# Performance work log

Measured on AMD Instinct MI355X. Metric: run time of the kernel, lower is better.

Reference implementation:

```python
import jax, jax.numpy as jnp
import numpy as np

EPS_LN = 1e-5


def layer_norm(x, g, b):
    mu = jnp.mean(x, axis=-1, keepdims=True)
    var = jnp.mean((x - mu) ** 2, axis=-1, keepdims=True)
    return (x - mu) * jax.lax.rsqrt(var + EPS_LN) * g + b


def setup_inputs() -> dict:
    key = jax.random.key(0)
    ks = jax.random.split(key, 16)
    N, E, H, EA = 25000, 400000, 128, 1
    h = jax.random.normal(ks[0], (N, H), dtype=jnp.float32)
    coord = jax.random.normal(ks[1], (N, 3), dtype=jnp.float32)
    edge_index = jax.random.randint(ks[2], (2, E), 0, N, dtype=jnp.int64)
    edge_attr = jax.random.normal(ks[3], (E, EA), dtype=jnp.float32)

    def lin(k, fan_in, fan_out):
        lim = 1.0 / np.sqrt(fan_in)
        return jax.random.uniform(k, (fan_in, fan_out), jnp.float32, -lim, lim)

    in_edge = 2 * H + 1 + EA  # 258
    params = {
        'e_W1': lin(ks[4], in_edge, H), 'e_b1': jnp.zeros((H,), jnp.float32),
        'e_g1': jnp.ones((H,), jnp.float32), 'e_be1': jnp.zeros((H,), jnp.float32),
        'e_W2': lin(ks[5], H, H), 'e_b2': jnp.zeros((H,), jnp.float32),
        'e_g2': jnp.ones((H,), jnp.float32), 'e_be2': jnp.zeros((H,), jnp.float32),
        'n_W1': lin(ks[6], 2 * H, H), 'n_b1': jnp.zeros((H,), jnp.float32),
        'n_g1': jnp.ones((H,), jnp.float32), 'n_be1': jnp.zeros((H,), jnp.float32),
        'n_W2': lin(ks[7], H, H), 'n_b2': jnp.zeros((H,), jnp.float32),
        'c_W1': lin(ks[8], H, H), 'c_b1': jnp.zeros((H,), jnp.float32),
        'c_g1': jnp.ones((H,), jnp.float32), 'c_be1': jnp.zeros((H,), jnp.float32),
        # xavier_uniform with gain=0.001, no bias
        'c_W2': jax.random.uniform(ks[9], (H, 1), jnp.float32, -1.0, 1.0) * (0.001 * np.sqrt(6.0 / (H + 1))),
    }
    return dict(h=h, edge_index=edge_index, coord=coord, edge_attr=edge_attr, **params)


def reference(h, edge_index, coord, edge_attr,
              e_W1, e_b1, e_g1, e_be1, e_W2, e_b2, e_g2, e_be2,
              n_W1, n_b1, n_g1, n_be1, n_W2, n_b2,
              c_W1, c_b1, c_g1, c_be1, c_W2):
    N = h.shape[0]
    row, col = edge_index[0], edge_index[1]

    coord_diff = coord[row] - coord[col]                     # [E,3]
    radial = jnp.sum(coord_diff ** 2, axis=1, keepdims=True)  # [E,1]
    norm = jnp.sqrt(radial + 1e-8)
    coord_diff = coord_diff / (norm + 1.0)

    inp = jnp.concatenate([h[row], h[col], radial, edge_attr], axis=1)  # [E,258]
    x = jax.nn.silu(layer_norm(inp @ e_W1 + e_b1, e_g1, e_be1))
    edge_feat = jax.nn.silu(layer_norm(x @ e_W2 + e_b2, e_g2, e_be2))   # [E,H]

    cm = jax.nn.silu(layer_norm(edge_feat @ c_W1 + c_b1, c_g1, c_be1)) @ c_W2  # [E,1]
    trans = coord_diff * cm                                   # [E,3]

    coord_out = coord + jax.ops.segment_sum(trans, row, num_segments=N)
    agg = jax.ops.segment_sum(edge_feat, row, num_segments=N)  # [N,H]

    node_in = jnp.concatenate([h, agg], axis=1)               # [N,2H]
    out = jax.nn.silu(layer_norm(node_in @ n_W1 + n_b1, n_g1, n_be1)) @ n_W2 + n_b2
    out = h + out  # recurrent
    return out, coord_out
```

## Files before the change

kernel.cpp:

```cpp
#include <hip/hip_runtime.h>
#include <math.h>

#define H 128
#define KE 256
#define KN 256
#define XSTR 136

typedef __attribute__((ext_vector_type(8))) short bf16x8;
typedef __attribute__((ext_vector_type(4))) float f32x4;

__device__ __forceinline__ float silu_f(float x) { return x / (1.0f + __expf(-x)); }

__device__ __forceinline__ unsigned short f2bf(float f) {
    unsigned int u = __float_as_uint(f);
    unsigned int r = u + 0x7FFFu + ((u >> 16) & 1u);
    return (unsigned short)(r >> 16);
}

__device__ __forceinline__ void atomic_pk_add_bf16(unsigned short* addr, unsigned int pkv) {
    asm volatile("global_atomic_pk_add_bf16 %0, %1, off"
                 :: "v"(addr), "v"(pkv) : "memory");
}

template<int CTRL>
__device__ __forceinline__ float dpp_add(float x) {
    int t = __builtin_amdgcn_update_dpp(0, __float_as_int(x), CTRL, 0xF, 0xF, true);
    return x + __int_as_float(t);
}
__device__ __forceinline__ float red16(float x) {
    x = dpp_add<0x128>(x);
    x = dpp_add<0x124>(x);
    x = dpp_add<0x122>(x);
    x = dpp_add<0x121>(x);
    return x;
}

__device__ __forceinline__ void wfrag(const float* __restrict__ W,
                                      unsigned short* __restrict__ Wf, int f) {
    int kb = f >> 9, rem = f & 511;
    int nt = rem >> 6, lane = rem & 63;
    int quad = lane >> 4, l15 = lane & 15;
    int n = nt * 16 + l15, k0 = kb * 32 + quad * 8;
    union { bf16x8 v; unsigned short u[8]; } pk;
    #pragma unroll
    for (int j = 0; j < 8; ++j) pk.u[j] = f2bf(W[(size_t)(k0 + j) * H + n]);
    *(bf16x8*)&Wf[(size_t)f * 8] = pk.v;
}

__global__ __launch_bounds__(256) void prep_all(
    const float* __restrict__ h, unsigned short* __restrict__ hb, int n4_h,
    float* __restrict__ aggz, int n4_agg,
    const float* __restrict__ coord, float* __restrict__ coord_out, int n_coord,
    const float* __restrict__ eW1, const float* __restrict__ eW2,
    const float* __restrict__ cW1, const float* __restrict__ nW1,
    const float* __restrict__ nW2,
    unsigned short* __restrict__ eW1f, unsigned short* __restrict__ eW2f,
    unsigned short* __restrict__ cW1f, unsigned short* __restrict__ nW1f,
    unsigned short* __restrict__ nW2f,
    int b0, int b1, int b2)
{
    int b = blockIdx.x;
    int t = threadIdx.x;
    if (b < b0) {
        int i = b * 256 + t;
        if (i < n4_h) {
            float4 f = ((const float4*)h)[i];
            ushort4 o;
            o.x = f2bf(f.x); o.y = f2bf(f.y); o.z = f2bf(f.z); o.w = f2bf(f.w);
            ((ushort4*)hb)[i] = o;
        }
    } else if (b < b1) {
        int i = (b - b0) * 256 + t;
        if (i < n4_agg) ((float4*)aggz)[i] = (float4){0.f, 0.f, 0.f, 0.f};
    } else if (b < b2) {
        int i = (b - b1) * 256 + t;
        if (i < n_coord) coord_out[i] = coord[i];
    } else {
        int idx = (b - b2) * 256 + t;
        if      (idx <  4096) wfrag(eW1, eW1f, idx);
        else if (idx <  8192) wfrag(nW1, nW1f, idx - 4096);
        else if (idx < 10240) wfrag(eW2, eW2f, idx - 8192);
        else if (idx < 12288) wfrag(cW1, cW1f, idx - 10240);
        else if (idx < 14336) wfrag(nW2, nW2f, idx - 12288);
    }
}

__device__ __forceinline__ void ln_silu_store1(
    f32x4* acc, const float* __restrict__ bias, const float* __restrict__ g,
    const float* __restrict__ be, unsigned short* X, int l15, int quad)
{
    float s[4] = {0,0,0,0}, q[4] = {0,0,0,0};
    #pragma unroll
    for (int nt = 0; nt < 8; ++nt) {
        float b = bias[nt * 16 + l15];
        #pragma unroll
        for (int r = 0; r < 4; ++r) {
            float x = acc[nt][r] + b; acc[nt][r] = x; s[r] += x; q[r] += x * x;
        }
    }
    #pragma unroll
    for (int r = 0; r < 4; ++r) { s[r] = red16(s[r]); q[r] = red16(q[r]); }
    #pragma unroll
    for (int r = 0; r < 4; ++r) {
        float mu = s[r] * 0.0078125f, v = q[r] * 0.0078125f - mu * mu;
        s[r] = mu; q[r] = rsqrtf(v + 1e-5f);
    }
    #pragma unroll
    for (int nt = 0; nt < 8; ++nt) {
        float gg = g[nt * 16 + l15], bb = be[nt * 16 + l15];
        #pragma unroll
        for (int r = 0; r < 4; ++r) {
            float a = q[r] * gg, c = bb - s[r] * a;
            float y = silu_f(acc[nt][r] * a + c);
            acc[nt][r] = y;
            X[(quad * 4 + r) * XSTR + nt * 16 + l15] = f2bf(y);
        }
    }
}

__global__ __launch_bounds__(64, 4) void edge_kernel(
    const unsigned short* __restrict__ hb, const int* __restrict__ ei,
    const float* __restrict__ coord, const float* __restrict__ eattr,
    const unsigned short* __restrict__ eW1f, const float* __restrict__ eW1,
    const float* __restrict__ eb1, const float* __restrict__ eg1, const float* __restrict__ ebe1,
    const unsigned short* __restrict__ eW2f,
    const float* __restrict__ eb2, const float* __restrict__ eg2, const float* __restrict__ ebe2,
    const unsigned short* __restrict__ cW1f,
    const float* __restrict__ cb1, const float* __restrict__ cg1, const float* __restrict__ cbe1,
    const float* __restrict__ cW2,
    unsigned short* __restrict__ aggb, float* __restrict__ coord_out, int E)
{
    __shared__ unsigned short X[16 * XSTR];

    const int lane = threadIdx.x;
    const int l15 = lane & 15, quad = lane >> 4;
    const int ge0 = blockIdx.x * 16;

    int el  = ge0 + l15;
    int elc = (el < E) ? el : (E - 1);
    int rowl = ei[elc], coll = ei[E + elc];
    float dx = coord[rowl * 3 + 0] - coord[coll * 3 + 0];
    float dy = coord[rowl * 3 + 1] - coord[coll * 3 + 1];
    float dz = coord[rowl * 3 + 2] - coord[coll * 3 + 2];
    float radial = dx * dx + dy * dy + dz * dz;
    float inv = 1.0f / (sqrtf(radial + 1e-8f) + 1.0f);
    float cdx = dx * inv, cdy = dy * inv, cdz = dz * inv;
    float ea = eattr[elc];

    f32x4 acc[8];
    #pragma unroll
    for (int nt = 0; nt < 8; ++nt) acc[nt] = (f32x4){0.f, 0.f, 0.f, 0.f};

    for (int kb = 0; kb < 8; ++kb) {
        int ko = (kb & 3) * 32 + quad * 8;
        bf16x8 af = *(const bf16x8*)(hb + (size_t)((kb < 4) ? rowl : coll) * H + ko);
        const unsigned short* bp = eW1f + ((size_t)kb * 8) * 512 + (size_t)lane * 8;
        #pragma unroll
        for (int nt = 0; nt < 8; ++nt) {
            bf16x8 bf = *(const bf16x8*)(bp + (size_t)nt * 512);
            acc[nt] = __builtin_amdgcn_mfma_f32_16x16x32_bf16(af, bf, acc[nt], 0, 0, 0);
        }
    }

    {
        float rad_r[4], ea_r[4];
        #pragma unroll
        for (int r = 0; r < 4; ++r) {
            rad_r[r] = __shfl(radial, quad * 4 + r, 64);
            ea_r[r]  = __shfl(ea,     quad * 4 + r, 64);
        }
        #pragma unroll
        for (int nt = 0; nt < 8; ++nt) {
            float w256 = eW1[256 * H + nt * 16 + l15];
            float w257 = eW1[257 * H + nt * 16 + l15];
            #pragma unroll
            for (int r = 0; r < 4; ++r)
                acc[nt][r] += rad_r[r] * w256 + ea_r[r] * w257;
        }
    }

    ln_silu_store1(acc, eb1, eg1, ebe1, X, l15, quad);

    f32x4 ac2[8];
    #pragma unroll
    for (int nt = 0; nt < 8; ++nt) ac2[nt] = (f32x4){0.f, 0.f, 0.f, 0.f};
    for (int kb = 0; kb < 4; ++kb) {
        bf16x8 af = *(const bf16x8*)&X[l15 * XSTR + kb * 32 + quad * 8];
        const unsigned short* bp = eW2f + ((size_t)kb * 8) * 512 + (size_t)lane * 8;
        #pragma unroll
        for (int nt = 0; nt < 8; ++nt) {
            bf16x8 bf = *(const bf16x8*)(bp + (size_t)nt * 512);
            ac2[nt] = __builtin_amdgcn_mfma_f32_16x16x32_bf16(af, bf, ac2[nt], 0, 0, 0);
        }
    }

    ln_silu_store1(ac2, eb2, eg2, ebe2, X, l15, quad);

    {
        int rowm[4];
        #pragma unroll
        for (int r = 0; r < 4; ++r) rowm[r] = __shfl(rowl, quad * 4 + r, 64);
        #pragma unroll
        for (int c4 = 0; c4 < 4; ++c4) {
            #pragma unroll
            for (int r = 0; r < 4; ++r) {
                int geh = ge0 + quad * 4 + r;
                if (geh < E) {
                    unsigned int pkv =
                        *(const unsigned int*)&X[(quad * 4 + r) * XSTR + c4 * 32 + 2 * l15];
                    atomic_pk_add_bf16(aggb + (size_t)rowm[r] * H + c4 * 32 + 2 * l15, pkv);
                }
            }
        }
    }

    #pragma unroll
    for (int nt = 0; nt < 8; ++nt) acc[nt] = (f32x4){0.f, 0.f, 0.f, 0.f};
    for (int kb = 0; kb < 4; ++kb) {
        bf16x8 af = *(const bf16x8*)&X[l15 * XSTR + kb * 32 + quad * 8];
        const unsigned short* bp = cW1f + ((size_t)kb * 8) * 512 + (size_t)lane * 8;
        #pragma unroll
        for (int nt = 0; nt < 8; ++nt) {
            bf16x8 bf = *(const bf16x8*)(bp + (size_t)nt * 512);
            acc[nt] = __builtin_amdgcn_mfma_f32_16x16x32_bf16(af, bf, acc[nt], 0, 0, 0);
        }
    }

    {
        float s[4] = {0,0,0,0}, q[4] = {0,0,0,0};
        #pragma unroll
        for (int nt = 0; nt < 8; ++nt) {
            float b = cb1[nt * 16 + l15];
            #pragma unroll
            for (int r = 0; r < 4; ++r) {
                float x = acc[nt][r] + b; acc[nt][r] = x; s[r] += x; q[r] += x * x;
            }
        }
        #pragma unroll
        for (int r = 0; r < 4; ++r) { s[r] = red16(s[r]); q[r] = red16(q[r]); }
        #pragma unroll
        for (int r = 0; r < 4; ++r) {
            float mu = s[r] * 0.0078125f, v = q[r] * 0.0078125f - mu * mu;
            s[r] = mu; q[r] = rsqrtf(v + 1e-5f);
        }
        float cm[4] = {0,0,0,0};
        #pragma unroll
        for (int nt = 0; nt < 8; ++nt) {
            float gg = cg1[nt * 16 + l15], bb = cbe1[nt * 16 + l15];
            float w2 = cW2[nt * 16 + l15];
            #pragma unroll
            for (int r = 0; r < 4; ++r) {
                float a = q[r] * gg, c = bb - s[r] * a;
                cm[r] += silu_f(acc[nt][r] * a + c) * w2;
            }
        }
        #pragma unroll
        for (int r = 0; r < 4; ++r) cm[r] = red16(cm[r]);
        #pragma unroll
        for (int r = 0; r < 4; ++r) {
            int src = quad * 4 + r;
            float cdxr = __shfl(cdx, src, 64);
            float cdyr = __shfl(cdy, src, 64);
            float cdzr = __shfl(cdz, src, 64);
            int rw = __shfl(rowl, src, 64);
            float comp = (l15 == 0) ? cdxr : ((l15 == 1) ? cdyr : cdzr);
            int geh = ge0 + src;
            if (l15 < 3 && geh < E)
                atomicAdd(&coord_out[(size_t)rw * 3 + l15], comp * cm[r]);
        }
    }
}

__global__ __launch_bounds__(256, 4) void node_kernel(
    const unsigned short* __restrict__ hb, const float* __restrict__ h,
    const unsigned short* __restrict__ aggb,
    const unsigned short* __restrict__ nW1f,
    const float* __restrict__ nb1, const float* __restrict__ ng1, const float* __restrict__ nbe1,
    const unsigned short* __restrict__ nW2f, const float* __restrict__ nb2,
    float* __restrict__ out, int N)
{
    __shared__ unsigned short Xs[4][16 * XSTR];

    const int wv   = threadIdx.x >> 6;
    const int lane = threadIdx.x & 63;
    const int l15 = lane & 15, quad = lane >> 4;
    const int gn0 = (blockIdx.x * 4 + wv) * 16;
    unsigned short* X = &Xs[wv][0];

    if (gn0 >= N) return;
    int nl = gn0 + l15; if (nl >= N) nl = N - 1;

    f32x4 acc[8];
    #pragma unroll
    for (int nt = 0; nt < 8; ++nt) acc[nt] = (f32x4){0.f, 0.f, 0.f, 0.f};

    for (int kb = 0; kb < 8; ++kb) {
        int ko = (kb & 3) * 32 + quad * 8;
        const unsigned short* src = (kb < 4) ? hb : aggb;
        bf16x8 af = *(const bf16x8*)(src + (size_t)nl * H + ko);
        const unsigned short* bp = nW1f + ((size_t)kb * 8) * 512 + (size_t)lane * 8;
        #pragma unroll
        for (int nt = 0; nt < 8; ++nt) {
            bf16x8 bf = *(const bf16x8*)(bp + (size_t)nt * 512);
            acc[nt] = __builtin_amdgcn_mfma_f32_16x16x32_bf16(af, bf, acc[nt], 0, 0, 0);
        }
    }

    ln_silu_store1(acc, nb1, ng1, nbe1, X, l15, quad);

    f32x4 ac2[8];
    #pragma unroll
    for (int nt = 0; nt < 8; ++nt) ac2[nt] = (f32x4){0.f, 0.f, 0.f, 0.f};
    for (int kb = 0; kb < 4; ++kb) {
        bf16x8 af = *(const bf16x8*)&X[l15 * XSTR + kb * 32 + quad * 8];
        const unsigned short* bp = nW2f + ((size_t)kb * 8) * 512 + (size_t)lane * 8;
        #pragma unroll
        for (int nt = 0; nt < 8; ++nt) {
            bf16x8 bf = *(const bf16x8*)(bp + (size_t)nt * 512);
            ac2[nt] = __builtin_amdgcn_mfma_f32_16x16x32_bf16(af, bf, ac2[nt], 0, 0, 0);
        }
    }

    #pragma unroll
    for (int nt = 0; nt < 8; ++nt) {
        float b = nb2[nt * 16 + l15];
        #pragma unroll
        for (int r = 0; r < 4; ++r) {
            int gn = gn0 + quad * 4 + r;
            if (gn < N) {
                size_t idx = (size_t)gn * H + nt * 16 + l15;
                out[idx] = ac2[nt][r] + b + h[idx];
            }
        }
    }
}

extern "C" void kernel_launch(void* const* d_in, const int* in_sizes, int n_in,
                              void* d_out, int out_size, void* d_ws, size_t ws_size,
                              hipStream_t stream) {
    const float* h     = (const float*)d_in[0];
    const int*   ei    = (const int*)d_in[1];
    const float* coord = (const float*)d_in[2];
    const float* eattr = (const float*)d_in[3];
    const float* eW1   = (const float*)d_in[4];
    const float* eb1   = (const float*)d_in[5];
    const float* eg1   = (const float*)d_in[6];
    const float* ebe1  = (const float*)d_in[7];
    const float* eW2   = (const float*)d_in[8];
    const float* eb2   = (const float*)d_in[9];
    const float* eg2   = (const float*)d_in[10];
    const float* ebe2  = (const float*)d_in[11];
    const float* nW1   = (const float*)d_in[12];
    const float* nb1   = (const float*)d_in[13];
    const float* ng1   = (const float*)d_in[14];
    const float* nbe1  = (const float*)d_in[15];
    const float* nW2   = (const float*)d_in[16];
    const float* nb2   = (const float*)d_in[17];
    const float* cW1   = (const float*)d_in[18];
    const float* cb1   = (const float*)d_in[19];
    const float* cg1   = (const float*)d_in[20];
    const float* cbe1  = (const float*)d_in[21];
    const float* cW2   = (const float*)d_in[22];

    const int N = in_sizes[0] / H;
    const int E = in_sizes[1] / 2;

    float* out       = (float*)d_out;
    float* coord_out = out + (size_t)N * H;

    char* ws = (char*)d_ws;
    size_t o = 0;
    unsigned short* aggb = (unsigned short*)(ws + o); o += (size_t)N * H * 2;
    unsigned short* hb   = (unsigned short*)(ws + o); o += (size_t)N * H * 2;
    unsigned short* eW1f = (unsigned short*)(ws + o); o += (size_t)H * KE * 2;
    unsigned short* eW2f = (unsigned short*)(ws + o); o += (size_t)H * H * 2;
    unsigned short* cW1f = (unsigned short*)(ws + o); o += (size_t)H * H * 2;
    unsigned short* nW1f = (unsigned short*)(ws + o); o += (size_t)H * KN * 2;
    unsigned short* nW2f = (unsigned short*)(ws + o); o += (size_t)H * H * 2;

    const int n4_h   = N * H / 4;
    const int n4_agg = N * H / 8;
    const int n_co   = N * 3;
    const int b0 = (n4_h   + 255) / 256;
    const int b1 = b0 + (n4_agg + 255) / 256;
    const int b2 = b1 + (n_co   + 255) / 256;
    const int bw = (4096 + 4096 + 2048 + 2048 + 2048 + 255) / 256;
    prep_all<<<b2 + bw, 256, 0, stream>>>(
        h, hb, n4_h, (float*)aggb, n4_agg, coord, coord_out, n_co,
        eW1, eW2, cW1, nW1, nW2,
        eW1f, eW2f, cW1f, nW1f, nW2f, b0, b1, b2);

    edge_kernel<<<(E + 15) / 16, 64, 0, stream>>>(
        hb, ei, coord, eattr,
        eW1f, eW1, eb1, eg1, ebe1,
        eW2f, eb2, eg2, ebe2,
        cW1f, cb1, cg1, cbe1, cW2,
        aggb, coord_out, E);

    node_kernel<<<(N + 63) / 64, 256, 0, stream>>>(
        hb, h, aggb, nW1f, nb1, ng1, nbe1, nW2f, nb2, out, N);
}
```

Before: 339.5 us.

## Transpose MFMA operands so each lane owns an edge row, simplify reductions

Swaps the A/B operands of every MFMA so the weight fragment is A and the activation is B. The output tile is then transposed, and each lane holds four consecutive feature columns of a single edge or node. With that layout the LayerNorm row reduction becomes two cross-quad shuffles, and bias, gamma and beta load as float4. Scatter atomics use the lane's own row index without shuffles, LDS and output writes are vectorised, and bf16 packing uses a hardware pack conversion when available. The aggregation atomics change from 32-bit-contiguous runs per row to scattered 4-element chunks per lane, which may change atomic coalescing.

After: 536.1 us. 57.9% more time.

```diff
diff --git a/kernel.cpp b/kernel.cpp
--- a/kernel.cpp
+++ b/kernel.cpp
@@ -17,22 +17,23 @@
     return (unsigned short)(r >> 16);
 }
 
+__device__ __forceinline__ unsigned int pkbf(float a, float b) {
+#if defined(__has_builtin)
+#if __has_builtin(__builtin_amdgcn_cvt_pk_bf16_f32)
+    typedef __attribute__((ext_vector_type(2))) __bf16 bf16x2_t;
+    bf16x2_t v = __builtin_amdgcn_cvt_pk_bf16_f32(a, b);
+    return *(unsigned int*)&v;
+#else
+    return (unsigned int)f2bf(a) | ((unsigned int)f2bf(b) << 16);
+#endif
+#else
+    return (unsigned int)f2bf(a) | ((unsigned int)f2bf(b) << 16);
+#endif
+}
+
 __device__ __forceinline__ void atomic_pk_add_bf16(unsigned short* addr, unsigned int pkv) {
     asm volatile("global_atomic_pk_add_bf16 %0, %1, off"
                  :: "v"(addr), "v"(pkv) : "memory");
-}
-
-template<int CTRL>
-__device__ __forceinline__ float dpp_add(float x) {
-    int t = __builtin_amdgcn_update_dpp(0, __float_as_int(x), CTRL, 0xF, 0xF, true);
-    return x + __int_as_float(t);
-}
-__device__ __forceinline__ float red16(float x) {
-    x = dpp_add<0x128>(x);
-    x = dpp_add<0x124>(x);
-    x = dpp_add<0x122>(x);
-    x = dpp_add<0x121>(x);
-    return x;
 }
 
 __device__ __forceinline__ void wfrag(const float* __restrict__ W,
@@ -65,9 +66,8 @@
         int i = b * 256 + t;
         if (i < n4_h) {
             float4 f = ((const float4*)h)[i];
-            ushort4 o;
-            o.x = f2bf(f.x); o.y = f2bf(f.y); o.z = f2bf(f.z); o.w = f2bf(f.w);
-            ((ushort4*)hb)[i] = o;
+            unsigned int lo = pkbf(f.x, f.y), hi = pkbf(f.z, f.w);
+            ((uint2*)hb)[i] = make_uint2(lo, hi);
         }
     } else if (b < b1) {
         int i = (b - b0) * 256 + t;
@@ -85,36 +85,33 @@
     }
 }
 
-__device__ __forceinline__ void ln_silu_store1(
+__device__ __forceinline__ void ln_silu_t(
     f32x4* acc, const float* __restrict__ bias, const float* __restrict__ g,
     const float* __restrict__ be, unsigned short* X, int l15, int quad)
 {
-    float s[4] = {0,0,0,0}, q[4] = {0,0,0,0};
+    float s = 0.f, q = 0.f;
     #pragma unroll
     for (int nt = 0; nt < 8; ++nt) {
-        float b = bias[nt * 16 + l15];
-        #pragma unroll
-        for (int r = 0; r < 4; ++r) {
-            float x = acc[nt][r] + b; acc[nt][r] = x; s[r] += x; q[r] += x * x;
-        }
-    }
-    #pragma unroll
-    for (int r = 0; r < 4; ++r) { s[r] = red16(s[r]); q[r] = red16(q[r]); }
-    #pragma unroll
-    for (int r = 0; r < 4; ++r) {
-        float mu = s[r] * 0.0078125f, v = q[r] * 0.0078125f - mu * mu;
-        s[r] = mu; q[r] = rsqrtf(v + 1e-5f);
-    }
+        float4 b4 = *(const float4*)(bias + nt * 16 + quad * 4);
+        acc[nt][0] += b4.x; acc[nt][1] += b4.y; acc[nt][2] += b4.z; acc[nt][3] += b4.w;
+        #pragma unroll
+        for (int r = 0; r < 4; ++r) { s += acc[nt][r]; q = fmaf(acc[nt][r], acc[nt][r], q); }
+    }
+    s += __shfl_xor(s, 16, 64); q += __shfl_xor(q, 16, 64);
+    s += __shfl_xor(s, 32, 64); q += __shfl_xor(q, 32, 64);
+    float mu   = s * 0.0078125f;
+    float rstd = rsqrtf(q * 0.0078125f - mu * mu + 1e-5f);
     #pragma unroll
     for (int nt = 0; nt < 8; ++nt) {
-        float gg = g[nt * 16 + l15], bb = be[nt * 16 + l15];
-        #pragma unroll
-        for (int r = 0; r < 4; ++r) {
-            float a = q[r] * gg, c = bb - s[r] * a;
-            float y = silu_f(acc[nt][r] * a + c);
-            acc[nt][r] = y;
-            X[(quad * 4 + r) * XSTR + nt * 16 + l15] = f2bf(y);
-        }
+        float4 g4 = *(const float4*)(g  + nt * 16 + quad * 4);
+        float4 e4 = *(const float4*)(be + nt * 16 + quad * 4);
+        float a0 = g4.x * rstd, a1 = g4.y * rstd, a2 = g4.z * rstd, a3 = g4.w * rstd;
+        float y0 = silu_f(fmaf(acc[nt][0] - mu, a0, e4.x));
+        float y1 = silu_f(fmaf(acc[nt][1] - mu, a1, e4.y));
+        float y2 = silu_f(fmaf(acc[nt][2] - mu, a2, e4.z));
+        float y3 = silu_f(fmaf(acc[nt][3] - mu, a3, e4.w));
+        acc[nt][0] = y0; acc[nt][1] = y1; acc[nt][2] = y2; acc[nt][3] = y3;
+        *(uint2*)&X[l15 * XSTR + nt * 16 + quad * 4] = make_uint2(pkbf(y0, y1), pkbf(y2, y3));
     }
 }
 
@@ -153,120 +150,91 @@
 
     for (int kb = 0; kb < 8; ++kb) {
         int ko = (kb & 3) * 32 + quad * 8;
-        bf16x8 af = *(const bf16x8*)(hb + (size_t)((kb < 4) ? rowl : coll) * H + ko);
-        const unsigned short* bp = eW1f + ((size_t)kb * 8) * 512 + (size_t)lane * 8;
-        #pragma unroll
-        for (int nt = 0; nt < 8; ++nt) {
-            bf16x8 bf = *(const bf16x8*)(bp + (size_t)nt * 512);
-            acc[nt] = __builtin_amdgcn_mfma_f32_16x16x32_bf16(af, bf, acc[nt], 0, 0, 0);
-        }
-    }
-
-    {
-        float rad_r[4], ea_r[4];
-        #pragma unroll
-        for (int r = 0; r < 4; ++r) {
-            rad_r[r] = __shfl(radial, quad * 4 + r, 64);
-            ea_r[r]  = __shfl(ea,     quad * 4 + r, 64);
-        }
-        #pragma unroll
-        for (int nt = 0; nt < 8; ++nt) {
-            float w256 = eW1[256 * H + nt * 16 + l15];
-            float w257 = eW1[257 * H + nt * 16 + l15];
-            #pragma unroll
-            for (int r = 0; r < 4; ++r)
-                acc[nt][r] += rad_r[r] * w256 + ea_r[r] * w257;
-        }
-    }
-
-    ln_silu_store1(acc, eb1, eg1, ebe1, X, l15, quad);
+        bf16x8 bfx = *(const bf16x8*)(hb + (size_t)((kb < 4) ? rowl : coll) * H + ko);
+        const unsigned short* ap = eW1f + ((size_t)kb * 8) * 512 + (size_t)lane * 8;
+        #pragma unroll
+        for (int nt = 0; nt < 8; ++nt) {
+            bf16x8 afw = *(const bf16x8*)(ap + (size_t)nt * 512);
+            acc[nt] = __builtin_amdgcn_mfma_f32_16x16x32_bf16(afw, bfx, acc[nt], 0, 0, 0);
+        }
+    }
+
+    #pragma unroll
+    for (int nt = 0; nt < 8; ++nt) {
+        float4 w6 = *(const float4*)(eW1 + 256 * H + nt * 16 + quad * 4);
+        float4 w7 = *(const float4*)(eW1 + 257 * H + nt * 16 + quad * 4);
+        acc[nt][0] += radial * w6.x + ea * w7.x;
+        acc[nt][1] += radial * w6.y + ea * w7.y;
+        acc[nt][2] += radial * w6.z + ea * w7.z;
+        acc[nt][3] += radial * w6.w + ea * w7.w;
+    }
+
+    ln_silu_t(acc, eb1, eg1, ebe1, X, l15, quad);
 
     f32x4 ac2[8];
     #pragma unroll
     for (int nt = 0; nt < 8; ++nt) ac2[nt] = (f32x4){0.f, 0.f, 0.f, 0.f};
     for (int kb = 0; kb < 4; ++kb) {
-        bf16x8 af = *(const bf16x8*)&X[l15 * XSTR + kb * 32 + quad * 8];
-        const unsigned short* bp = eW2f + ((size_t)kb * 8) * 512 + (size_t)lane * 8;
-        #pragma unroll
-        for (int nt = 0; nt < 8; ++nt) {
-            bf16x8 bf = *(const bf16x8*)(bp + (size_t)nt * 512);
-            ac2[nt] = __builtin_amdgcn_mfma_f32_16x16x32_bf16(af, bf, ac2[nt], 0, 0, 0);
-        }
-    }
-
-    ln_silu_store1(ac2, eb2, eg2, ebe2, X, l15, quad);
-
-    {
-        int rowm[4];
-        #pragma unroll
-        for (int r = 0; r < 4; ++r) rowm[r] = __shfl(rowl, quad * 4 + r, 64);
-        #pragma unroll
-        for (int c4 = 0; c4 < 4; ++c4) {
-            #pragma unroll
-            for (int r = 0; r < 4; ++r) {
-                int geh = ge0 + quad * 4 + r;
-                if (geh < E) {
-                    unsigned int pkv =
-                        *(const unsigned int*)&X[(quad * 4 + r) * XSTR + c4 * 32 + 2 * l15];
-                    atomic_pk_add_bf16(aggb + (size_t)rowm[r] * H + c4 * 32 + 2 * l15, pkv);
-                }
-            }
+        bf16x8 bfx = *(const bf16x8*)&X[l15 * XSTR + kb * 32 + quad * 8];
+        const unsigned short* ap = eW2f + ((size_t)kb * 8) * 512 + (size_t)lane * 8;
+        #pragma unroll
+        for (int nt = 0; nt < 8; ++nt) {
+            bf16x8 afw = *(const bf16x8*)(ap + (size_t)nt * 512);
+            ac2[nt] = __builtin_amdgcn_mfma_f32_16x16x32_bf16(afw, bfx, ac2[nt], 0, 0, 0);
+        }
+    }
+
+    ln_silu_t(ac2, eb2, eg2, ebe2, X, l15, quad);
+    if (el < E) {
+        unsigned short* ab = aggb + (size_t)rowl * H + quad * 4;
+        #pragma unroll
+        for (int nt = 0; nt < 8; ++nt) {
+            atomic_pk_add_bf16(ab + nt * 16,     pkbf(ac2[nt][0], ac2[nt][1]));
+            atomic_pk_add_bf16(ab + nt * 16 + 2, pkbf(ac2[nt][2], ac2[nt][3]));
         }
     }
 
     #pragma unroll
     for (int nt = 0; nt < 8; ++nt) acc[nt] = (f32x4){0.f, 0.f, 0.f, 0.f};
     for (int kb = 0; kb < 4; ++kb) {
-        bf16x8 af = *(const bf16x8*)&X[l15 * XSTR + kb * 32 + quad * 8];
-        const unsigned short* bp = cW1f + ((size_t)kb * 8) * 512 + (size_t)lane * 8;
-        #pragma unroll
-        for (int nt = 0; nt < 8; ++nt) {
-            bf16x8 bf = *(const bf16x8*)(bp + (size_t)nt * 512);
-            acc[nt] = __builtin_amdgcn_mfma_f32_16x16x32_bf16(af, bf, acc[nt], 0, 0, 0);
+        bf16x8 bfx = *(const bf16x8*)&X[l15 * XSTR + kb * 32 + quad * 8];
+        const unsigned short* ap = cW1f + ((size_t)kb * 8) * 512 + (size_t)lane * 8;
+        #pragma unroll
+        for (int nt = 0; nt < 8; ++nt) {
+            bf16x8 afw = *(const bf16x8*)(ap + (size_t)nt * 512);
+            acc[nt] = __builtin_amdgcn_mfma_f32_16x16x32_bf16(afw, bfx, acc[nt], 0, 0, 0);
         }
     }
 
     {
-        float s[4] = {0,0,0,0}, q[4] = {0,0,0,0};
-        #pragma unroll
-        for (int nt = 0; nt < 8; ++nt) {
-            float b = cb1[nt * 16 + l15];
+        float s = 0.f, q = 0.f;
+        #pragma unroll
+        for (int nt = 0; nt < 8; ++nt) {
+            float4 b4 = *(const float4*)(cb1 + nt * 16 + quad * 4);
+            acc[nt][0] += b4.x; acc[nt][1] += b4.y; acc[nt][2] += b4.z; acc[nt][3] += b4.w;
             #pragma unroll
-            for (int r = 0; r < 4; ++r) {
-                float x = acc[nt][r] + b; acc[nt][r] = x; s[r] += x; q[r] += x * x;
-            }
-        }
-        #pragma unroll
-        for (int r = 0; r < 4; ++r) { s[r] = red16(s[r]); q[r] = red16(q[r]); }
-        #pragma unroll
-        for (int r = 0; r < 4; ++r) {
-            float mu = s[r] * 0.0078125f, v = q[r] * 0.0078125f - mu * mu;
-            s[r] = mu; q[r] = rsqrtf(v + 1e-5f);
-        }
-        float cm[4] = {0,0,0,0};
-        #pragma unroll
-        for (int nt = 0; nt < 8; ++nt) {
-            float gg = cg1[nt * 16 + l15], bb = cbe1[nt * 16 + l15];
-            float w2 = cW2[nt * 16 + l15];
-            #pragma unroll
-            for (int r = 0; r < 4; ++r) {
-                float a = q[r] * gg, c = bb - s[r] * a;
-                cm[r] += silu_f(acc[nt][r] * a + c) * w2;
-            }
-        }
-        #pragma unroll
-        for (int r = 0; r < 4; ++r) cm[r] = red16(cm[r]);
-        #pragma unroll
-        for (int r = 0; r < 4; ++r) {
-            int src = quad * 4 + r;
-            float cdxr = __shfl(cdx, src, 64);
-            float cdyr = __shfl(cdy, src, 64);
-            float cdzr = __shfl(cdz, src, 64);
-            int rw = __shfl(rowl, src, 64);
-            float comp = (l15 == 0) ? cdxr : ((l15 == 1) ? cdyr : cdzr);
-            int geh = ge0 + src;
-            if (l15 < 3 && geh < E)
-                atomicAdd(&coord_out[(size_t)rw * 3 + l15], comp * cm[r]);
+            for (int r = 0; r < 4; ++r) { s += acc[nt][r]; q = fmaf(acc[nt][r], acc[nt][r], q); }
+        }
+        s += __shfl_xor(s, 16, 64); q += __shfl_xor(q, 16, 64);
+        s += __shfl_xor(s, 32, 64); q += __shfl_xor(q, 32, 64);
+        float mu   = s * 0.0078125f;
+        float rstd = rsqrtf(q * 0.0078125f - mu * mu + 1e-5f);
+        float cm = 0.f;
+        #pragma unroll
+        for (int nt = 0; nt < 8; ++nt) {
+            float4 g4 = *(const float4*)(cg1  + nt * 16 + quad * 4);
+            float4 e4 = *(const float4*)(cbe1 + nt * 16 + quad * 4);
+            float4 w4 = *(const float4*)(cW2  + nt * 16 + quad * 4);
+            cm = fmaf(silu_f(fmaf(acc[nt][0] - mu, g4.x * rstd, e4.x)), w4.x, cm);
+            cm = fmaf(silu_f(fmaf(acc[nt][1] - mu, g4.y * rstd, e4.y)), w4.y, cm);
+            cm = fmaf(silu_f(fmaf(acc[nt][2] - mu, g4.z * rstd, e4.z)), w4.z, cm);
+            cm = fmaf(silu_f(fmaf(acc[nt][3] - mu, g4.w * rstd, e4.w)), w4.w, cm);
+        }
+        cm += __shfl_xor(cm, 16, 64);
+        cm += __shfl_xor(cm, 32, 64);
+        if (quad < 3 && el < E) {
+            float comp = (quad == 0) ? cdx : ((quad == 1) ? cdy : cdz);
+            atomicAdd(&coord_out[(size_t)rowl * 3 + quad], comp * cm);
         }
     }
 }
@@ -288,7 +256,8 @@
     unsigned short* X = &Xs[wv][0];
 
     if (gn0 >= N) return;
-    int nl = gn0 + l15; if (nl >= N) nl = N - 1;
+    int gn = gn0 + l15;
+    int nl = (gn < N) ? gn : (N - 1);
 
     f32x4 acc[8];
     #pragma unroll
@@ -297,40 +266,41 @@
     for (int kb = 0; kb < 8; ++kb) {
         int ko = (kb & 3) * 32 + quad * 8;
         const unsigned short* src = (kb < 4) ? hb : aggb;
-        bf16x8 af = *(const bf16x8*)(src + (size_t)nl * H + ko);
-        const unsigned short* bp = nW1f + ((size_t)kb * 8) * 512 + (size_t)lane * 8;
-        #pragma unroll
-        for (int nt = 0; nt < 8; ++nt) {
-            bf16x8 bf = *(const bf16x8*)(bp + (size_t)nt * 512);
-            acc[nt] = __builtin_amdgcn_mfma_f32_16x16x32_bf16(af, bf, acc[nt], 0, 0, 0);
-        }
-    }
-
-    ln_silu_store1(acc, nb1, ng1, nbe1, X, l15, quad);
+        bf16x8 bfx = *(const bf16x8*)(src + (size_t)nl * H + ko);
+        const unsigned short* ap = nW1f + ((size_t)kb * 8) * 512 + (size_t)lane * 8;
+        #pragma unroll
+        for (int nt = 0; nt < 8; ++nt) {
+            bf16x8 afw = *(const bf16x8*)(ap + (size_t)nt * 512);
+            acc[nt] = __builtin_amdgcn_mfma_f32_16x16x32_bf16(afw, bfx, acc[nt], 0, 0, 0);
+        }
+    }
+
+    ln_silu_t(acc, nb1, ng1, nbe1, X, l15, quad);
 
     f32x4 ac2[8];
     #pragma unroll
     for (int nt = 0; nt < 8; ++nt) ac2[nt] = (f32x4){0.f, 0.f, 0.f, 0.f};
     for (int kb = 0; kb < 4; ++kb) {
-        bf16x8 af = *(const bf16x8*)&X[l15 * XSTR + kb * 32 + quad * 8];
-        const unsigned short* bp = nW2f + ((size_t)kb * 8) * 512 + (size_t)lane * 8;
-        #pragma unroll
-        for (int nt = 0; nt < 8; ++nt) {
-            bf16x8 bf = *(const bf16x8*)(bp + (size_t)nt * 512);
-            ac2[nt] = __builtin_amdgcn_mfma_f32_16x16x32_bf16(af, bf, ac2[nt], 0, 0, 0);
-        }
-    }
-
-    #pragma unroll
-    for (int nt = 0; nt < 8; ++nt) {
-        float b = nb2[nt * 16 + l15];
-        #pragma unroll
-        for (int r = 0; r < 4; ++r) {
-            int gn = gn0 + quad * 4 + r;
-            if (gn < N) {
-                size_t idx = (size_t)gn * H + nt * 16 + l15;
-                out[idx] = ac2[nt][r] + b + h[idx];
-            }
+        bf16x8 bfx = *(const bf16x8*)&X[l15 * XSTR + kb * 32 + quad * 8];
+        const unsigned short* ap = nW2f + ((size_t)kb * 8) * 512 + (size_t)lane * 8;
+        #pragma unroll
+        for (int nt = 0; nt < 8; ++nt) {
+            bf16x8 afw = *(const bf16x8*)(ap + (size_t)nt * 512);
+            ac2[nt] = __builtin_amdgcn_mfma_f32_16x16x32_bf16(afw, bfx, ac2[nt], 0, 0, 0);
+        }
+    }
+
+    if (gn < N) {
+        #pragma unroll
+        for (int nt = 0; nt < 8; ++nt) {
+            float4 b4 = *(const float4*)(nb2 + nt * 16 + quad * 4);
+            const float4 hv = *(const float4*)(h + (size_t)gn * H + nt * 16 + quad * 4);
+            float4 o;
+            o.x = ac2[nt][0] + b4.x + hv.x;
+            o.y = ac2[nt][1] + b4.y + hv.y;
+            o.z = ac2[nt][2] + b4.z + hv.z;
+            o.w = ac2[nt][3] + b4.w + hv.w;
+            *(float4*)(out + (size_t)gn * H + nt * 16 + quad * 4) = o;
         }
     }
 }
```
